# Performance work log

Measured on AMD Instinct MI355X. Metric: run time of the kernel, lower is better.

Reference implementation:

```python
import jax, jax.numpy as jnp
import numpy as np

B, M, N = 262144, 3, 256   # batch, soil layers, runoff features
H1, H2 = 256, 128          # MLP hidden widths (layer_units[:-1]); last layer is scalar


def setup_inputs() -> dict:
    key = jax.random.key(0)
    ks = jax.random.split(key, 9)
    runoff = jax.random.uniform(ks[0], (B, M, N), dtype=jnp.float32)
    last_flow = jax.random.uniform(ks[1], (B, M), dtype=jnp.float32)
    last_free_water = jax.random.uniform(ks[2], (B, M), dtype=jnp.float32)
    s = 0.05
    # m independent tiny MLPs, stacked along leading axis m
    W1 = jax.random.normal(ks[3], (M, N, H1), dtype=jnp.float32) * s
    b1 = jnp.zeros((M, H1), dtype=jnp.float32)
    W2 = jax.random.normal(ks[4], (M, H1, H2), dtype=jnp.float32) * s
    b2 = jnp.zeros((M, H2), dtype=jnp.float32)
    W3 = jax.random.normal(ks[5], (M, H2), dtype=jnp.float32) * s  # last layer has 1 unit
    b3 = jnp.zeros((M,), dtype=jnp.float32)
    return {
        "last_flow": last_flow,
        "last_free_water": last_free_water,
        "runoff": runoff,
        "W1": W1, "b1": b1, "W2": W2, "b2": b2, "W3": W3, "b3": b3,
    }


def reference(last_flow, last_free_water, runoff, W1, b1, W2, b2, W3, b3):
    # step 1: add summed runoff to free-water state  (B, M)
    free_water = last_free_water + jnp.sum(runoff, axis=-1)
    # step 2: m small MLPs -> per-layer outflow ratio in (0,1), batched over m via einsum
    a1 = jax.nn.relu(jnp.einsum('bmn,mnh->bmh', runoff, W1) + b1)        # (B, M, H1)
    a2 = jax.nn.relu(jnp.einsum('bmh,mhk->bmk', a1, W2) + b2)            # (B, M, H2)
    ratio = jax.nn.sigmoid(jnp.einsum('bmk,mk->bm', a2, W3) + b3)        # (B, M)
    # step 3: blend free water with previous flow
    flow = free_water * ratio + last_flow * (1.0 - ratio)
    # step 4: update free-water state
    new_free_water = free_water - flow
    return (new_free_water, flow)
```

## Files before the change

kernel.cpp:

```cpp
#include <hip/hip_runtime.h>
#include <hip/hip_bf16.h>


#define B_TOT 262144
#define M_    3
#define N_    256
#define H1_   256
#define H2_   128
#define BM_   (B_TOT * M_)

typedef __bf16 bf16_t;
typedef __bf16  bf16x8 __attribute__((ext_vector_type(8)));
typedef float   f32x16 __attribute__((ext_vector_type(16)));
typedef float   f32x4  __attribute__((ext_vector_type(4)));

__device__ __forceinline__ unsigned pack_bf2(float lo, float hi) {
  union { bf16_t b; unsigned short u; } a, c;
  a.b = (bf16_t)lo; c.b = (bf16_t)hi;
  return ((unsigned)c.u << 16) | (unsigned)a.u;
}

__device__ __forceinline__ void gload_lds16(const void* g, void* l) {
  __builtin_amdgcn_global_load_lds(
      (const __attribute__((address_space(1))) void*)g,
      (__attribute__((address_space(3))) void*)l, 16, 0, 0);
}

__global__ __launch_bounds__(256) void prep_weights(
    const float* __restrict__ W1, const float* __restrict__ W2,
    bf16_t* __restrict__ w1s, bf16_t* __restrict__ w2s)
{
  int id = blockIdx.x * 256 + threadIdx.x;
  const int NW1 = M_ * 16 * 8 * 64;
  const int NW2 = M_ * 16 * 4 * 64;
  if (id < NW1) {
    int lane = id & 63;
    int t    = (id >> 6) & 7;
    int kk   = (id >> 9) & 15;
    int m    = id >> 13;
    int h  = 32 * t + (lane & 31);
    int n0 = 16 * kk + 8 * (lane >> 5);
    bf16x8 v;
#pragma unroll
    for (int ii = 0; ii < 8; ++ii)
      v[ii] = (bf16_t)W1[((size_t)m * N_ + (n0 + ii)) * H1_ + h];
    *reinterpret_cast<bf16x8*>(&w1s[(size_t)id * 8]) = v;
  } else if (id < NW1 + NW2) {
    int j    = id - NW1;
    int lane = j & 63;
    int t2   = (j >> 6) & 3;
    int kk2  = (j >> 8) & 15;
    int m    = j >> 12;
    int k2 = 32 * t2 + (lane & 31);
    int h0 = 16 * kk2 + 8 * (lane >> 5);
    bf16x8 v;
#pragma unroll
    for (int ii = 0; ii < 8; ++ii)
      v[ii] = (bf16_t)W2[((size_t)m * H1_ + (h0 + ii)) * H2_ + k2];
    *reinterpret_cast<bf16x8*>(&w2s[(size_t)j * 8]) = v;
  }
}

__global__ __launch_bounds__(256, 2) void reservoir_kernel(
    const float* __restrict__ last_flow,
    const float* __restrict__ last_fw,
    const float* __restrict__ runoff,
    const float* __restrict__ b1,
    const float* __restrict__ b2,
    const float* __restrict__ W3,
    const float* __restrict__ b3,
    const bf16_t* __restrict__ w1s,
    const bf16_t* __restrict__ w2s,
    float* __restrict__ out)
{
  __shared__ alignas(16) float  sR[2][128 * 32];
  __shared__ alignas(16) bf16_t sW1[2][8192];
  __shared__ alignas(16) bf16_t sW2[2][2048];
  __shared__ alignas(16) float  sB1[H1_];
  __shared__ alignas(16) float  sB2[H2_];
  __shared__ alignas(16) float  sW3[H2_];

  const int tid  = threadIdx.x;
  const int lane = tid & 63;
  const int wv   = tid >> 6;
  const int m    = blockIdx.y;
  const int hi   = lane >> 5;
  const int r    = lane & 31;
  const int r7   = r & 7;
  const int row0 = blockIdx.x * 128;
  const int row  = row0 + wv * 32 + r;

  const int l3 = lane >> 3;
  const int gsw = (lane & 7) ^ l3;

  const bf16_t* w1base = w1s + (size_t)m * 65536;
  const bf16_t* w2base = w2s + (size_t)m * 32768;

  auto stage_R = [&](int g, int buf) {
#pragma unroll
    for (int c = 0; c < 4; ++c) {
      int slab = wv * 4 + c;
      const float* src = runoff
          + ((size_t)(row0 + slab * 8 + l3) * M_ + m) * N_ + 32 * g + 4 * gsw;
      gload_lds16(src, &sR[buf][slab * 256]);
    }
  };
  auto stage_w1g = [&](int g, int buf) {
#pragma unroll
    for (int c = 0; c < 4; ++c) {
      int chunk = wv * 4 + c;
      gload_lds16(w1base + (size_t)g * 8192 + chunk * 512 + lane * 8,
                  &sW1[buf][chunk * 512]);
    }
  };
  auto stage_w2 = [&](int kk2, int buf) {
    gload_lds16(w2base + (size_t)kk2 * 2048 + wv * 512 + lane * 8,
                &sW2[buf][wv * 512]);
  };

  sB1[tid] = b1[m * H1_ + tid];
  if (tid < H2_) { sB2[tid] = b2[m * H2_ + tid]; sW3[tid] = W3[m * H2_ + tid]; }
  stage_R(0, 0);
  stage_w1g(0, 0);
  __syncthreads();

  f32x16 acc1[8];
#pragma unroll
  for (int t = 0; t < 8; ++t) {
#pragma unroll
    for (int g2 = 0; g2 < 4; ++g2) {
      f32x4 bv = *reinterpret_cast<const f32x4*>(&sB1[32 * t + 8 * g2 + 4 * hi]);
      acc1[t][4 * g2 + 0] = bv[0];
      acc1[t][4 * g2 + 1] = bv[1];
      acc1[t][4 * g2 + 2] = bv[2];
      acc1[t][4 * g2 + 3] = bv[3];
    }
  }

  float rsum = 0.f;
  const float* rrow_base_off = nullptr; (void)rrow_base_off;

#pragma unroll
  for (int g = 0; g < 8; ++g) {
    const int cb = g & 1;
    if (g < 7) { stage_R(g + 1, cb ^ 1); stage_w1g(g + 1, cb ^ 1); }
    else       { stage_w2(0, 0); }

#pragma unroll
    for (int q = 0; q < 2; ++q) {
      const float* rb = &sR[cb][(wv * 32 + r) * 32];
      f32x4 qa = *reinterpret_cast<const f32x4*>(&rb[((4 * q + 2 * hi + 0) ^ r7) * 4]);
      f32x4 qb = *reinterpret_cast<const f32x4*>(&rb[((4 * q + 2 * hi + 1) ^ r7) * 4]);
      rsum += qa[0] + qa[1] + qa[2] + qa[3] + qb[0] + qb[1] + qb[2] + qb[3];
      bf16x8 bfrag;
      bfrag[0] = (bf16_t)qa[0]; bfrag[1] = (bf16_t)qa[1];
      bfrag[2] = (bf16_t)qa[2]; bfrag[3] = (bf16_t)qa[3];
      bfrag[4] = (bf16_t)qb[0]; bfrag[5] = (bf16_t)qb[1];
      bfrag[6] = (bf16_t)qb[2]; bfrag[7] = (bf16_t)qb[3];

#pragma unroll
      for (int t = 0; t < 8; ++t) {
        bf16x8 afrag = *reinterpret_cast<const bf16x8*>(
            &sW1[cb][q * 4096 + t * 512 + lane * 8]);
        acc1[t] = __builtin_amdgcn_mfma_f32_32x32x16_bf16(afrag, bfrag, acc1[t], 0, 0, 0);
      }
    }
    __syncthreads();
  }

  unsigned P[8][2][2][2];
#pragma unroll
  for (int t = 0; t < 8; ++t)
#pragma unroll
    for (int q = 0; q < 2; ++q)
#pragma unroll
      for (int v = 0; v < 2; ++v)
#pragma unroll
        for (int s = 0; s < 2; ++s) {
          int e = 8 * q + 4 * v + 2 * s;
          P[t][q][v][s] = pack_bf2(fmaxf(acc1[t][e], 0.f),
                                   fmaxf(acc1[t][e + 1], 0.f));
        }

  f32x16 acc2[4];
#pragma unroll
  for (int t2 = 0; t2 < 4; ++t2) {
#pragma unroll
    for (int g2 = 0; g2 < 4; ++g2) {
      f32x4 bv = *reinterpret_cast<const f32x4*>(&sB2[32 * t2 + 8 * g2 + 4 * hi]);
      acc2[t2][4 * g2 + 0] = bv[0];
      acc2[t2][4 * g2 + 1] = bv[1];
      acc2[t2][4 * g2 + 2] = bv[2];
      acc2[t2][4 * g2 + 3] = bv[3];
    }
  }

#pragma unroll
  for (int kk2 = 0; kk2 < 16; ++kk2) {
    const int cb = kk2 & 1;
    if (kk2 < 15) stage_w2(kk2 + 1, cb ^ 1);
    const int t = kk2 >> 1, q = kk2 & 1;

    auto r0 = __builtin_amdgcn_permlane32_swap(P[t][q][0][0], P[t][q][1][0], false, false);
    auto r1 = __builtin_amdgcn_permlane32_swap(P[t][q][0][1], P[t][q][1][1], false, false);
    union { unsigned u[4]; bf16x8 v; } bb;
    bb.u[0] = r0[0]; bb.u[1] = r1[0]; bb.u[2] = r0[1]; bb.u[3] = r1[1];

#pragma unroll
    for (int t2 = 0; t2 < 4; ++t2) {
      bf16x8 afrag = *reinterpret_cast<const bf16x8*>(
          &sW2[cb][t2 * 512 + lane * 8]);
      acc2[t2] = __builtin_amdgcn_mfma_f32_32x32x16_bf16(afrag, bb.v, acc2[t2], 0, 0, 0);
    }
    __syncthreads();
  }

  float part = 0.f;
#pragma unroll
  for (int t2 = 0; t2 < 4; ++t2) {
#pragma unroll
    for (int g2 = 0; g2 < 4; ++g2) {
      f32x4 w3v = *reinterpret_cast<const f32x4*>(&sW3[32 * t2 + 8 * g2 + 4 * hi]);
      part += fmaxf(acc2[t2][4 * g2 + 0], 0.f) * w3v[0]
            + fmaxf(acc2[t2][4 * g2 + 1], 0.f) * w3v[1]
            + fmaxf(acc2[t2][4 * g2 + 2], 0.f) * w3v[2]
            + fmaxf(acc2[t2][4 * g2 + 3], 0.f) * w3v[3];
    }
  }
  part += __shfl_xor(part, 32, 64);
  rsum += __shfl_xor(rsum, 32, 64);

  const float x     = part + b3[m];
  const float ratio = 1.0f / (1.0f + __expf(-x));
  const size_t oi   = (size_t)row * M_ + m;
  const float fw    = last_fw[oi] + rsum;
  const float lf    = last_flow[oi];
  const float flow  = fw * ratio + lf * (1.0f - ratio);
  if (hi == 0) {
    out[oi]        = fw - flow;
    out[BM_ + oi]  = flow;
  }
}

extern "C" void kernel_launch(void* const* d_in, const int* in_sizes, int n_in,
                              void* d_out, int out_size, void* d_ws, size_t ws_size,
                              hipStream_t stream) {
  const float* last_flow = (const float*)d_in[0];
  const float* last_fw   = (const float*)d_in[1];
  const float* runoff    = (const float*)d_in[2];
  const float* W1 = (const float*)d_in[3];
  const float* b1 = (const float*)d_in[4];
  const float* W2 = (const float*)d_in[5];
  const float* b2 = (const float*)d_in[6];
  const float* W3 = (const float*)d_in[7];
  const float* b3 = (const float*)d_in[8];
  float* out = (float*)d_out;

  bf16_t* w1s = (bf16_t*)d_ws;
  bf16_t* w2s = w1s + (size_t)M_ * 65536;

  prep_weights<<<144, 256, 0, stream>>>(W1, W2, w1s, w2s);

  dim3 grid(B_TOT / 128, M_);
  reservoir_kernel<<<grid, 256, 0, stream>>>(last_flow, last_fw, runoff,
                                             b1, b2, W3, b3, w1s, w2s, out);
}
```

Before: 289.1 us.

## Make reservoir kernel persistent with deeper runoff pipeline and resident W2

Replaces the one-tile-per-block grid with 768 blocks that each process 8 consecutive 128-row tiles for one soil layer. A continuous cross-tile prefetch stream uses triple-buffered runoff and double-buffered W1, with manual vmcnt waits and raw barriers. All of W2 is loaded into LDS once per block, removing the per-step W2 staging and barriers in layer 2. This amortises per-block setup and keeps loads in flight across tile boundaries, at the cost of larger LDS use, occupancy reduced to 1 block per CU, and fragile hand-counted wait counts.

```diff
diff --git a/kernel.cpp b/kernel.cpp
--- a/kernel.cpp
+++ b/kernel.cpp
@@ -61,7 +61,7 @@
   }
 }
 
-__global__ __launch_bounds__(256, 2) void reservoir_kernel(
+__global__ __launch_bounds__(256, 1) void reservoir_kernel(
     const float* __restrict__ last_flow,
     const float* __restrict__ last_fw,
     const float* __restrict__ runoff,
@@ -73,9 +73,9 @@
     const bf16_t* __restrict__ w2s,
     float* __restrict__ out)
 {
-  __shared__ alignas(16) float  sR[2][128 * 32];
+  __shared__ alignas(16) float  sR[3][128 * 32];
   __shared__ alignas(16) bf16_t sW1[2][8192];
-  __shared__ alignas(16) bf16_t sW2[2][2048];
+  __shared__ alignas(16) bf16_t sW2[16 * 2048];
   __shared__ alignas(16) float  sB1[H1_];
   __shared__ alignas(16) float  sB2[H2_];
   __shared__ alignas(16) float  sW3[H2_];
@@ -83,162 +83,170 @@
   const int tid  = threadIdx.x;
   const int lane = tid & 63;
   const int wv   = tid >> 6;
-  const int m    = blockIdx.y;
   const int hi   = lane >> 5;
   const int r    = lane & 31;
   const int r7   = r & 7;
-  const int row0 = blockIdx.x * 128;
-  const int row  = row0 + wv * 32 + r;
-
-  const int l3 = lane >> 3;
-  const int gsw = (lane & 7) ^ l3;
+  const int l3   = lane >> 3;
+  const int gsw  = (lane & 7) ^ l3;
+
+  const int bidx  = blockIdx.x;
+  const int m     = bidx >> 8;
+  const int rbase = (bidx & 255) * 1024;
 
   const bf16_t* w1base = w1s + (size_t)m * 65536;
   const bf16_t* w2base = w2s + (size_t)m * 32768;
 
-  auto stage_R = [&](int g, int buf) {
+  auto stage_R = [&](int ai) {
+    int aic  = ai < 63 ? ai : 63;
+    int row0 = rbase + (aic >> 3) * 128;
+    int g    = aic & 7;
+    float* dst = &sR[ai % 3][0];
 #pragma unroll
     for (int c = 0; c < 4; ++c) {
       int slab = wv * 4 + c;
       const float* src = runoff
           + ((size_t)(row0 + slab * 8 + l3) * M_ + m) * N_ + 32 * g + 4 * gsw;
-      gload_lds16(src, &sR[buf][slab * 256]);
+      gload_lds16(src, dst + slab * 256);
     }
   };
-  auto stage_w1g = [&](int g, int buf) {
+  auto stage_W1 = [&](int wai) {
+    int g = wai & 7;
+    bf16_t* dst = &sW1[wai & 1][0];
 #pragma unroll
     for (int c = 0; c < 4; ++c) {
       int chunk = wv * 4 + c;
       gload_lds16(w1base + (size_t)g * 8192 + chunk * 512 + lane * 8,
-                  &sW1[buf][chunk * 512]);
+                  dst + chunk * 512);
     }
   };
-  auto stage_w2 = [&](int kk2, int buf) {
-    gload_lds16(w2base + (size_t)kk2 * 2048 + wv * 512 + lane * 8,
-                &sW2[buf][wv * 512]);
-  };
-
+
+  stage_R(0);  stage_W1(0);
+  stage_R(1);  stage_W1(1);
+  stage_R(2);
+#pragma unroll
+  for (int i = 0; i < 16; ++i) {
+    int chunk = wv * 16 + i;
+    gload_lds16(w2base + (size_t)chunk * 512 + lane * 8, &sW2[chunk * 512]);
+  }
   sB1[tid] = b1[m * H1_ + tid];
   if (tid < H2_) { sB2[tid] = b2[m * H2_ + tid]; sW3[tid] = W3[m * H2_ + tid]; }
-  stage_R(0, 0);
-  stage_w1g(0, 0);
   __syncthreads();
 
-  f32x16 acc1[8];
-#pragma unroll
-  for (int t = 0; t < 8; ++t) {
-#pragma unroll
-    for (int g2 = 0; g2 < 4; ++g2) {
-      f32x4 bv = *reinterpret_cast<const f32x4*>(&sB1[32 * t + 8 * g2 + 4 * hi]);
-      acc1[t][4 * g2 + 0] = bv[0];
-      acc1[t][4 * g2 + 1] = bv[1];
-      acc1[t][4 * g2 + 2] = bv[2];
-      acc1[t][4 * g2 + 3] = bv[3];
-    }
-  }
-
-  float rsum = 0.f;
-  const float* rrow_base_off = nullptr; (void)rrow_base_off;
-
-#pragma unroll
-  for (int g = 0; g < 8; ++g) {
-    const int cb = g & 1;
-    if (g < 7) { stage_R(g + 1, cb ^ 1); stage_w1g(g + 1, cb ^ 1); }
-    else       { stage_w2(0, 0); }
-
-#pragma unroll
-    for (int q = 0; q < 2; ++q) {
-      const float* rb = &sR[cb][(wv * 32 + r) * 32];
-      f32x4 qa = *reinterpret_cast<const f32x4*>(&rb[((4 * q + 2 * hi + 0) ^ r7) * 4]);
-      f32x4 qb = *reinterpret_cast<const f32x4*>(&rb[((4 * q + 2 * hi + 1) ^ r7) * 4]);
-      rsum += qa[0] + qa[1] + qa[2] + qa[3] + qb[0] + qb[1] + qb[2] + qb[3];
-      bf16x8 bfrag;
-      bfrag[0] = (bf16_t)qa[0]; bfrag[1] = (bf16_t)qa[1];
-      bfrag[2] = (bf16_t)qa[2]; bfrag[3] = (bf16_t)qa[3];
-      bfrag[4] = (bf16_t)qb[0]; bfrag[5] = (bf16_t)qb[1];
-      bfrag[6] = (bf16_t)qb[2]; bfrag[7] = (bf16_t)qb[3];
-
-#pragma unroll
-      for (int t = 0; t < 8; ++t) {
+  for (int u = 0; u < 8; ++u) {
+    const int row = rbase + u * 128 + wv * 32 + r;
+
+    f32x16 acc1[8];
+#pragma unroll
+    for (int t = 0; t < 8; ++t) {
+#pragma unroll
+      for (int g2 = 0; g2 < 4; ++g2) {
+        f32x4 bv = *reinterpret_cast<const f32x4*>(&sB1[32 * t + 8 * g2 + 4 * hi]);
+        acc1[t][4 * g2 + 0] = bv[0];
+        acc1[t][4 * g2 + 1] = bv[1];
+        acc1[t][4 * g2 + 2] = bv[2];
+        acc1[t][4 * g2 + 3] = bv[3];
+      }
+    }
+    float rsum = 0.f;
+
+    for (int g = 0; g < 8; ++g) {
+      const int ai = u * 8 + g;
+      asm volatile("s_waitcnt vmcnt(8)" ::: "memory");
+      __builtin_amdgcn_sched_barrier(0);
+      __builtin_amdgcn_s_barrier();
+
+      const float*  rp = &sR[ai % 3][(wv * 32 + r) * 32];
+      const bf16_t* wp = &sW1[ai & 1][0];
+#pragma unroll
+      for (int q = 0; q < 2; ++q) {
+        f32x4 qa = *reinterpret_cast<const f32x4*>(&rp[((4 * q + 2 * hi + 0) ^ r7) * 4]);
+        f32x4 qb = *reinterpret_cast<const f32x4*>(&rp[((4 * q + 2 * hi + 1) ^ r7) * 4]);
+        rsum += qa[0] + qa[1] + qa[2] + qa[3] + qb[0] + qb[1] + qb[2] + qb[3];
+        bf16x8 bfrag;
+        bfrag[0] = (bf16_t)qa[0]; bfrag[1] = (bf16_t)qa[1];
+        bfrag[2] = (bf16_t)qa[2]; bfrag[3] = (bf16_t)qa[3];
+        bfrag[4] = (bf16_t)qb[0]; bfrag[5] = (bf16_t)qb[1];
+        bfrag[6] = (bf16_t)qb[2]; bfrag[7] = (bf16_t)qb[3];
+#pragma unroll
+        for (int t = 0; t < 8; ++t) {
+          bf16x8 afrag = *reinterpret_cast<const bf16x8*>(
+              &wp[q * 4096 + t * 512 + lane * 8]);
+          acc1[t] = __builtin_amdgcn_mfma_f32_32x32x16_bf16(afrag, bfrag, acc1[t], 0, 0, 0);
+        }
+      }
+
+      __builtin_amdgcn_s_barrier();
+      stage_R(ai + 3);
+      stage_W1(ai + 2);
+    }
+
+    unsigned P[8][2][2][2];
+#pragma unroll
+    for (int t = 0; t < 8; ++t)
+#pragma unroll
+      for (int q = 0; q < 2; ++q)
+#pragma unroll
+        for (int v = 0; v < 2; ++v)
+#pragma unroll
+          for (int s = 0; s < 2; ++s) {
+            int e = 8 * q + 4 * v + 2 * s;
+            P[t][q][v][s] = pack_bf2(fmaxf(acc1[t][e], 0.f),
+                                     fmaxf(acc1[t][e + 1], 0.f));
+          }
+
+    f32x16 acc2[4];
+#pragma unroll
+    for (int t2 = 0; t2 < 4; ++t2) {
+#pragma unroll
+      for (int g2 = 0; g2 < 4; ++g2) {
+        f32x4 bv = *reinterpret_cast<const f32x4*>(&sB2[32 * t2 + 8 * g2 + 4 * hi]);
+        acc2[t2][4 * g2 + 0] = bv[0];
+        acc2[t2][4 * g2 + 1] = bv[1];
+        acc2[t2][4 * g2 + 2] = bv[2];
+        acc2[t2][4 * g2 + 3] = bv[3];
+      }
+    }
+
+#pragma unroll
+    for (int kk2 = 0; kk2 < 16; ++kk2) {
+      const int t = kk2 >> 1, q = kk2 & 1;
+      auto r0 = __builtin_amdgcn_permlane32_swap(P[t][q][0][0], P[t][q][1][0], false, false);
+      auto r1 = __builtin_amdgcn_permlane32_swap(P[t][q][0][1], P[t][q][1][1], false, false);
+      union { unsigned uu[4]; bf16x8 v; } bb;
+      bb.uu[0] = r0[0]; bb.uu[1] = r1[0]; bb.uu[2] = r0[1]; bb.uu[3] = r1[1];
+#pragma unroll
+      for (int t2 = 0; t2 < 4; ++t2) {
         bf16x8 afrag = *reinterpret_cast<const bf16x8*>(
-            &sW1[cb][q * 4096 + t * 512 + lane * 8]);
-        acc1[t] = __builtin_amdgcn_mfma_f32_32x32x16_bf16(afrag, bfrag, acc1[t], 0, 0, 0);
-      }
-    }
-    __syncthreads();
-  }
-
-  unsigned P[8][2][2][2];
-#pragma unroll
-  for (int t = 0; t < 8; ++t)
-#pragma unroll
-    for (int q = 0; q < 2; ++q)
-#pragma unroll
-      for (int v = 0; v < 2; ++v)
-#pragma unroll
-        for (int s = 0; s < 2; ++s) {
-          int e = 8 * q + 4 * v + 2 * s;
-          P[t][q][v][s] = pack_bf2(fmaxf(acc1[t][e], 0.f),
-                                   fmaxf(acc1[t][e + 1], 0.f));
-        }
-
-  f32x16 acc2[4];
-#pragma unroll
-  for (int t2 = 0; t2 < 4; ++t2) {
-#pragma unroll
-    for (int g2 = 0; g2 < 4; ++g2) {
-      f32x4 bv = *reinterpret_cast<const f32x4*>(&sB2[32 * t2 + 8 * g2 + 4 * hi]);
-      acc2[t2][4 * g2 + 0] = bv[0];
-      acc2[t2][4 * g2 + 1] = bv[1];
-      acc2[t2][4 * g2 + 2] = bv[2];
-      acc2[t2][4 * g2 + 3] = bv[3];
-    }
-  }
-
-#pragma unroll
-  for (int kk2 = 0; kk2 < 16; ++kk2) {
-    const int cb = kk2 & 1;
-    if (kk2 < 15) stage_w2(kk2 + 1, cb ^ 1);
-    const int t = kk2 >> 1, q = kk2 & 1;
-
-    auto r0 = __builtin_amdgcn_permlane32_swap(P[t][q][0][0], P[t][q][1][0], false, false);
-    auto r1 = __builtin_amdgcn_permlane32_swap(P[t][q][0][1], P[t][q][1][1], false, false);
-    union { unsigned u[4]; bf16x8 v; } bb;
-    bb.u[0] = r0[0]; bb.u[1] = r1[0]; bb.u[2] = r0[1]; bb.u[3] = r1[1];
-
+            &sW2[kk2 * 2048 + t2 * 512 + lane * 8]);
+        acc2[t2] = __builtin_amdgcn_mfma_f32_32x32x16_bf16(afrag, bb.v, acc2[t2], 0, 0, 0);
+      }
+    }
+
+    float part = 0.f;
 #pragma unroll
     for (int t2 = 0; t2 < 4; ++t2) {
-      bf16x8 afrag = *reinterpret_cast<const bf16x8*>(
-          &sW2[cb][t2 * 512 + lane * 8]);
-      acc2[t2] = __builtin_amdgcn_mfma_f32_32x32x16_bf16(afrag, bb.v, acc2[t2], 0, 0, 0);
-    }
-    __syncthreads();
-  }
-
-  float part = 0.f;
-#pragma unroll
-  for (int t2 = 0; t2 < 4; ++t2) {
-#pragma unroll
-    for (int g2 = 0; g2 < 4; ++g2) {
-      f32x4 w3v = *reinterpret_cast<const f32x4*>(&sW3[32 * t2 + 8 * g2 + 4 * hi]);
-      part += fmaxf(acc2[t2][4 * g2 + 0], 0.f) * w3v[0]
-            + fmaxf(acc2[t2][4 * g2 + 1], 0.f) * w3v[1]
-            + fmaxf(acc2[t2][4 * g2 + 2], 0.f) * w3v[2]
-            + fmaxf(acc2[t2][4 * g2 + 3], 0.f) * w3v[3];
-    }
-  }
-  part += __shfl_xor(part, 32, 64);
-  rsum += __shfl_xor(rsum, 32, 64);
-
-  const float x     = part + b3[m];
-  const float ratio = 1.0f / (1.0f + __expf(-x));
-  const size_t oi   = (size_t)row * M_ + m;
-  const float fw    = last_fw[oi] + rsum;
-  const float lf    = last_flow[oi];
-  const float flow  = fw * ratio + lf * (1.0f - ratio);
-  if (hi == 0) {
-    out[oi]        = fw - flow;
-    out[BM_ + oi]  = flow;
+#pragma unroll
+      for (int g2 = 0; g2 < 4; ++g2) {
+        f32x4 w3v = *reinterpret_cast<const f32x4*>(&sW3[32 * t2 + 8 * g2 + 4 * hi]);
+        part += fmaxf(acc2[t2][4 * g2 + 0], 0.f) * w3v[0]
+              + fmaxf(acc2[t2][4 * g2 + 1], 0.f) * w3v[1]
+              + fmaxf(acc2[t2][4 * g2 + 2], 0.f) * w3v[2]
+              + fmaxf(acc2[t2][4 * g2 + 3], 0.f) * w3v[3];
+      }
+    }
+    part += __shfl_xor(part, 32, 64);
+    rsum += __shfl_xor(rsum, 32, 64);
+
+    const float x     = part + b3[m];
+    const float ratio = 1.0f / (1.0f + __expf(-x));
+    const size_t oi   = (size_t)row * M_ + m;
+    const float fw    = last_fw[oi] + rsum;
+    const float lf    = last_flow[oi];
+    const float flow  = fw * ratio + lf * (1.0f - ratio);
+    if (hi == 0) {
+      out[oi]        = fw - flow;
+      out[BM_ + oi]  = flow;
+    }
   }
 }
 
@@ -261,7 +269,6 @@
 
   prep_weights<<<144, 256, 0, stream>>>(W1, W2, w1s, w2s);
 
-  dim3 grid(B_TOT / 128, M_);
-  reservoir_kernel<<<grid, 256, 0, stream>>>(last_flow, last_fw, runoff,
-                                             b1, b2, W3, b3, w1s, w2s, out);
-}
+  reservoir_kernel<<<768, 256, 0, stream>>>(last_flow, last_fw, runoff,
+                                            b1, b2, W3, b3, w1s, w2s, out);
+}
```

New measurement: 284.9 us. No clear change (-1.4%).
